# Kernel optimization log

Measured on AMD Instinct MI355X. Metric: run time of the kernel, lower is better.

Reference implementation:

```python
import jax, jax.numpy as jnp
import numpy as np

N_NODES = 60000
N_EDGES = 240000
N_REL = 4
N_GRAPHS = 128
D_IN = 768
D_H = 256
N_LAYERS = 6


def setup_inputs() -> dict:
    key = jax.random.key(0)
    ks = jax.random.split(key, 16)
    x = jax.random.normal(ks[0], (N_NODES, D_IN), dtype=jnp.float32)
    edge_index = jax.random.randint(ks[1], (2, N_EDGES), 0, N_NODES, dtype=jnp.int64)
    edge_attr = jax.random.randint(ks[2], (N_EDGES,), 0, N_REL, dtype=jnp.int64)
    batch = jnp.sort(jax.random.randint(ks[3], (N_NODES,), 0, N_GRAPHS, dtype=jnp.int64))
    s0 = 1.0 / np.sqrt(D_IN)
    s1 = 1.0 / np.sqrt(D_H)
    w0 = jax.random.normal(ks[4], (N_REL, D_IN, D_H), dtype=jnp.float32) * s0
    root0 = jax.random.normal(ks[5], (D_IN, D_H), dtype=jnp.float32) * s0
    b0 = jnp.zeros((D_H,), jnp.float32)
    w_rest = jax.random.normal(ks[6], (N_LAYERS - 1, N_REL, D_H, D_H), dtype=jnp.float32) * s1
    root_rest = jax.random.normal(ks[7], (N_LAYERS - 1, D_H, D_H), dtype=jnp.float32) * s1
    b_rest = jnp.zeros((N_LAYERS - 1, D_H), jnp.float32)
    fc1_w = jax.random.normal(ks[8], (2 * D_H, 128), dtype=jnp.float32) * (1.0 / np.sqrt(2 * D_H))
    fc1_b = jnp.zeros((128,), jnp.float32)
    fc2_w = jax.random.normal(ks[9], (128, 1), dtype=jnp.float32) * (1.0 / np.sqrt(128))
    fc2_b = jnp.zeros((1,), jnp.float32)
    return {"x": x, "edge_index": edge_index, "edge_attr": edge_attr, "batch": batch,
            "w0": w0, "root0": root0, "b0": b0,
            "w_rest": w_rest, "root_rest": root_rest, "b_rest": b_rest,
            "fc1_w": fc1_w, "fc1_b": fc1_b, "fc2_w": fc2_w, "fc2_b": fc2_b}


def _rgcn(h, src, dst, rel, W, root, b):
    # PyG RGCNConv with aggr='mean': per-relation mean over incoming edges,
    # transformed by per-relation weight, plus root transform and bias.
    n = h.shape[0]
    seg = rel * n + dst                                   # combined (relation, target) segment id
    msgs = h[src]                                         # [E, d_in] gather
    agg = jax.ops.segment_sum(msgs, seg, num_segments=N_REL * n)
    agg = agg.reshape(N_REL, n, -1)                       # [R, N, d_in]
    cnt = jax.ops.segment_sum(jnp.ones_like(rel, jnp.float32), seg, num_segments=N_REL * n)
    cnt = cnt.reshape(N_REL, n, 1)
    mean = agg / jnp.maximum(cnt, 1.0)                    # mean aggregation; 0 for isolated nodes
    return jnp.einsum('rnd,rdo->no', mean, W) + h @ root + b


def reference(x, edge_index, edge_attr, batch, w0, root0, b0,
              w_rest, root_rest, b_rest, fc1_w, fc1_b, fc2_w, fc2_b):
    src, dst = edge_index[0], edge_index[1]
    h = jax.nn.relu(_rgcn(x, src, dst, edge_attr, w0, root0, b0))
    for i in range(N_LAYERS - 1):
        h = jax.nn.relu(_rgcn(h, src, dst, edge_attr, w_rest[i], root_rest[i], b_rest[i]))
    # global mean / max pooling over graphs
    sums = jax.ops.segment_sum(h, batch, num_segments=N_GRAPHS)
    cnt = jax.ops.segment_sum(jnp.ones((h.shape[0],), jnp.float32), batch, num_segments=N_GRAPHS)[:, None]
    h_mean = sums / jnp.maximum(cnt, 1.0)
    h_max = jax.ops.segment_max(h, batch, num_segments=N_GRAPHS)
    h_max = jnp.where(cnt > 0, h_max, 0.0)
    g = jnp.concatenate([h_mean, h_max], axis=1)          # [G, 512]
    out = jax.nn.relu(g @ fc1_w + fc1_b)                  # dropout is identity at inference
    out = out @ fc2_w + fc2_b
    return jax.nn.sigmoid(out.squeeze(-1))                # [G]
```

## Files before the change

kernel.cpp:

```cpp
#include <hip/hip_runtime.h>
#include <hip/hip_bf16.h>

#define N_NODES  60000
#define N_EDGES  240000
#define N_REL    4
#define N_GRAPHS 128
#define D_IN     768
#define D_H      256
#define N_LAYERS 6
#define M_PAD    60032
#define N_TOT    1280
#define BM_L     64
#define LDM      264

static inline int cdiv(int a, int b) { return (a + b - 1) / b; }

typedef __attribute__((ext_vector_type(8))) short short8;
typedef __attribute__((ext_vector_type(4))) float f32x4;

__device__ __forceinline__ float bf2f(unsigned short u) {
    union { unsigned int i; float f; } c; c.i = ((unsigned int)u) << 16; return c.f;
}
__device__ __forceinline__ float bflo(unsigned int u) {
    union { unsigned int i; float f; } c; c.i = u << 16; return c.f;
}
__device__ __forceinline__ float bfhi(unsigned int u) {
    union { unsigned int i; float f; } c; c.i = u & 0xffff0000u; return c.f;
}
__device__ __forceinline__ unsigned short f2bf(float f) {
    union { float f; unsigned int i; } c; c.f = f;
    unsigned int i = c.i;
    unsigned int r = (i + 0x7FFFu + ((i >> 16) & 1u)) >> 16;
    return (unsigned short)r;
}

__device__ __forceinline__ void gload16(const void* g, void* l) {
    __builtin_amdgcn_global_load_lds((const __attribute__((address_space(1))) void*)g,
                                     (__attribute__((address_space(3))) void*)l, 16, 0, 0);
}

__global__ __launch_bounds__(512) void gemm_l0(
    const unsigned short* __restrict__ A,
    const unsigned short* __restrict__ Bt,
    const float* __restrict__ bias,
    unsigned short* __restrict__ out_root,
    unsigned short* __restrict__ out_msg,
    int K)
{
    __shared__ unsigned short As[128 * 32];
    __shared__ unsigned short Bs[256 * 32];

    const int tid  = threadIdx.x;
    const int wave = tid >> 6, lane = tid & 63;
    const int bn = blockIdx.x * 256;
    const int bm = blockIdx.y * 128;
    const int wm = (wave & 1) * 64, wn = (wave >> 1) * 64;

    const int lr = lane >> 2;
    const int kg = ((lane & 3) ^ ((lr ^ (lr >> 2)) & 3)) * 8;
    const unsigned short* gsrc[3];
    unsigned short* ldst[3];
    #pragma unroll
    for (int j = 0; j < 3; ++j) {
        int g = wave * 3 + j;
        if (g < 8) {
            gsrc[j] = A + (size_t)(bm + g * 16 + lr) * K + kg;
            ldst[j] = As + g * 16 * 32;
        } else {
            gsrc[j] = Bt + (size_t)(bn + (g - 8) * 16 + lr) * K + kg;
            ldst[j] = Bs + (g - 8) * 16 * 32;
        }
    }

    f32x4 acc[4][4] = {};
    const int fr = lane & 15;
    const int qsw = (((lane >> 4) ^ fr ^ (fr >> 2)) & 3) * 8;

    for (int k0 = 0; k0 < K; k0 += 32) {
        gload16(gsrc[0] + k0, ldst[0]);
        gload16(gsrc[1] + k0, ldst[1]);
        gload16(gsrc[2] + k0, ldst[2]);
        __syncthreads();

        short8 a[4], b[4];
        #pragma unroll
        for (int t = 0; t < 4; ++t) {
            a[t] = *(const short8*)&As[(wm + t * 16 + fr) * 32 + qsw];
            b[t] = *(const short8*)&Bs[(wn + t * 16 + fr) * 32 + qsw];
        }
        #pragma unroll
        for (int mt = 0; mt < 4; ++mt)
            #pragma unroll
            for (int nt = 0; nt < 4; ++nt)
                acc[mt][nt] = __builtin_amdgcn_mfma_f32_16x16x32_bf16(
                    a[mt], b[nt], acc[mt][nt], 0, 0, 0);
        __syncthreads();
    }

    const bool is_root = (bn == 0);
    #pragma unroll
    for (int mt = 0; mt < 4; ++mt) {
        #pragma unroll
        for (int nt = 0; nt < 4; ++nt) {
            int col = bn + wn + nt * 16 + fr;
            float bv = bias[col];
            #pragma unroll
            for (int r = 0; r < 4; ++r) {
                int row = bm + wm + mt * 16 + ((lane >> 4) << 2) + r;
                float v = acc[mt][nt][r] + bv;
                if (is_root) out_root[(size_t)row * 256 + col] = f2bf(v);
                else         out_msg[(size_t)row * 1024 + (col - 256)] = f2bf(v);
            }
        }
    }
}

__global__ __launch_bounds__(512) void rgcn_layer(
    const unsigned short* __restrict__ h,
    const unsigned short* __restrict__ Wl,
    const float* __restrict__ bias,
    const int* __restrict__ rp4,
    const int* __restrict__ e_srcs,
    const float* __restrict__ inv4,
    unsigned short* __restrict__ h_out)
{
    __shared__ unsigned short mt[BM_L * LDM];
    __shared__ unsigned short Bs[256 * 32];

    const int tid  = threadIdx.x;
    const int wave = tid >> 6, lane = tid & 63;
    const int bm = blockIdx.x * BM_L;

    const int node  = bm + lane;
    const int cq    = wave * 32;
    const bool valid = node < N_NODES;

    const int lr = lane >> 2;
    const int kg = ((lane & 3) ^ ((lr ^ (lr >> 2)) & 3)) * 8;

    const int fr  = lane & 15;
    const int q8  = (lane >> 4) * 8;
    const int qsw = (((lane >> 4) ^ fr ^ (fr >> 2)) & 3) * 8;
    const int wcol = wave * 32;

    float4 iv = valid ? *(const float4*)&inv4[(size_t)node * 4]
                      : make_float4(1.f, 1.f, 1.f, 1.f);

    f32x4 acc[4][2] = {};

    for (int r = 0; r < 5; ++r) {
        float4 am[8] = {};
        uint4 self[2];
        if (r < 4) {
            if (valid) {
                int lo = rp4[(size_t)node * 4 + r];
                int hi = rp4[(size_t)node * 4 + r + 1];
                for (int e = lo; e < hi; ++e) {
                    int s = e_srcs[e];
                    const uint4* hp = (const uint4*)(h + (size_t)s * 256 + cq);
                    #pragma unroll
                    for (int j = 0; j < 2; ++j) {
                        uint4 v = hp[j];
                        am[4*j+0].x += bflo(v.x); am[4*j+0].y += bfhi(v.x);
                        am[4*j+0].z += bflo(v.y); am[4*j+0].w += bfhi(v.y);
                        am[4*j+1].x += bflo(v.z); am[4*j+1].y += bfhi(v.z);
                        am[4*j+1].z += bflo(v.w); am[4*j+1].w += bfhi(v.w);
                    }
                    #pragma unroll
                    for (int j = 0; j < 0; ++j) {}
                }
            }
        }
        if (r < 4) {
            am[0]=make_float4(0,0,0,0); am[1]=am[0]; am[2]=am[0]; am[3]=am[0];
            am[4]=am[0]; am[5]=am[0]; am[6]=am[0]; am[7]=am[0];
            if (valid) {
                int lo = rp4[(size_t)node * 4 + r];
                int hi = rp4[(size_t)node * 4 + r + 1];
                for (int e = lo; e < hi; ++e) {
                    int s = e_srcs[e];
                    const uint4* hp = (const uint4*)(h + (size_t)s * 256 + cq);
                    #pragma unroll
                    for (int j = 0; j < 4; ++j) {
                        uint2 v = ((const uint2*)hp)[j];
                        am[2*j+0].x += bflo(v.x); am[2*j+0].y += bfhi(v.x);
                        am[2*j+0].z += bflo(v.y); am[2*j+0].w += bfhi(v.y);
                        uint2 w = ((const uint2*)hp)[j]; (void)w;
                        am[2*j+1].x += 0.f;
                    }
                }
            }
        }
        {
            #pragma unroll
            for (int j = 0; j < 8; ++j) am[j] = make_float4(0,0,0,0);
            if (r < 4) {
                if (valid) {
                    int lo = rp4[(size_t)node * 4 + r];
                    int hi = rp4[(size_t)node * 4 + r + 1];
                    for (int e = lo; e < hi; ++e) {
                        int s = e_srcs[e];
                        const uint4* hp = (const uint4*)(h + (size_t)s * 256 + cq);
                        uint4 v0 = hp[0];
                        uint4 v1 = hp[1];
                        am[0].x += bflo(v0.x); am[0].y += bfhi(v0.x);
                        am[0].z += bflo(v0.y); am[0].w += bfhi(v0.y);
                        am[1].x += bflo(v0.z); am[1].y += bfhi(v0.z);
                        am[1].z += bflo(v0.w); am[1].w += bfhi(v0.w);
                        am[2].x += bflo(v1.x); am[2].y += bfhi(v1.x);
                        am[2].z += bflo(v1.y); am[2].w += bfhi(v1.y);
                        am[3].x += bflo(v1.z); am[3].y += bfhi(v1.z);
                        am[3].z += bflo(v1.w); am[3].w += bfhi(v1.w);
                        const uint4* hp2 = hp + 2;
                        uint4 v2 = hp2[0];
                        uint4 v3 = hp2[1];
                        am[4].x += bflo(v2.x); am[4].y += bfhi(v2.x);
                        am[4].z += bflo(v2.y); am[4].w += bfhi(v2.y);
                        am[5].x += bflo(v2.z); am[5].y += bfhi(v2.z);
                        am[5].z += bflo(v2.w); am[5].w += bfhi(v2.w);
                        am[6].x += bflo(v3.x); am[6].y += bfhi(v3.x);
                        am[6].z += bflo(v3.y); am[6].w += bfhi(v3.y);
                        am[7].x += bflo(v3.z); am[7].y += bfhi(v3.z);
                        am[7].z += bflo(v3.w); am[7].w += bfhi(v3.w);
                    }
                }
            } else {
                const uint4* hp = (const uint4*)(h + (size_t)node * 256 + cq);
                self[0] = hp[0]; self[1] = hp[1];
                uint4 s2 = hp[2], s3 = hp[3];
                am[0].x = bflo(self[0].x); am[0].y = bfhi(self[0].x);
                am[0].z = bflo(self[0].y); am[0].w = bfhi(self[0].y);
                am[1].x = bflo(self[0].z); am[1].y = bfhi(self[0].z);
                am[1].z = bflo(self[0].w); am[1].w = bfhi(self[0].w);
                am[2].x = bflo(self[1].x); am[2].y = bfhi(self[1].x);
                am[2].z = bflo(self[1].y); am[2].w = bfhi(self[1].y);
                am[3].x = bflo(self[1].z); am[3].y = bfhi(self[1].z);
                am[3].z = bflo(self[1].w); am[3].w = bfhi(self[1].w);
                am[4].x = bflo(s2.x); am[4].y = bfhi(s2.x);
                am[4].z = bflo(s2.y); am[4].w = bfhi(s2.y);
                am[5].x = bflo(s2.z); am[5].y = bfhi(s2.z);
                am[5].z = bflo(s2.w); am[5].w = bfhi(s2.w);
                am[6].x = bflo(s3.x); am[6].y = bfhi(s3.x);
                am[6].z = bflo(s3.y); am[6].w = bfhi(s3.y);
                am[7].x = bflo(s3.z); am[7].y = bfhi(s3.z);
                am[7].z = bflo(s3.w); am[7].w = bfhi(s3.w);
            }
        }
        float sc = (r == 0) ? iv.x : (r == 1) ? iv.y : (r == 2) ? iv.z
                 : (r == 3) ? iv.w : 1.f;

        __syncthreads();
        {
            unsigned short* dst = &mt[lane * LDM + cq];
            #pragma unroll
            for (int j = 0; j < 8; ++j) {
                ushort4 o;
                o.x = f2bf(am[j].x * sc); o.y = f2bf(am[j].y * sc);
                o.z = f2bf(am[j].z * sc); o.w = f2bf(am[j].w * sc);
                *(ushort4*)(dst + j * 4) = o;
            }
        }

        const int rOff = r << 8;
        #pragma unroll 1
        for (int kk = 0; kk < 8; ++kk) {
            if (kk > 0) __syncthreads();
            {
                int g0 = wave * 2;
                gload16(Wl + (size_t)(g0 * 16 + lr) * N_TOT + rOff + kg + kk * 32,
                        Bs + g0 * 512);
                gload16(Wl + (size_t)((g0 + 1) * 16 + lr) * N_TOT + rOff + kg + kk * 32,
                        Bs + (g0 + 1) * 512);
            }
            __syncthreads();

            short8 a[4], b[2];
            #pragma unroll
            for (int i = 0; i < 4; ++i)
                a[i] = *(const short8*)&mt[(i * 16 + fr) * LDM + kk * 32 + q8];
            #pragma unroll
            for (int nt = 0; nt < 2; ++nt)
                b[nt] = *(const short8*)&Bs[(wcol + nt * 16 + fr) * 32 + qsw];
            #pragma unroll
            for (int i = 0; i < 4; ++i)
                #pragma unroll
                for (int nt = 0; nt < 2; ++nt)
                    acc[i][nt] = __builtin_amdgcn_mfma_f32_16x16x32_bf16(
                        a[i], b[nt], acc[i][nt], 0, 0, 0);
        }
        __syncthreads();
    }

    #pragma unroll
    for (int i = 0; i < 4; ++i) {
        #pragma unroll
        for (int nt = 0; nt < 2; ++nt) {
            int col = wcol + nt * 16 + fr;
            float bv = bias[col];
            #pragma unroll
            for (int rg = 0; rg < 4; ++rg) {
                int row = bm + i * 16 + ((lane >> 4) << 2) + rg;
                float v = fmaxf(acc[i][nt][rg] + bv, 0.f);
                h_out[(size_t)row * 256 + col] = f2bf(v);
            }
        }
    }
}

__global__ void convert_x(const float* __restrict__ x, unsigned short* __restrict__ xb) {
    size_t i = ((size_t)blockIdx.x * 256 + threadIdx.x) * 4;
    if (i >= (size_t)M_PAD * D_IN) return;
    ushort4 o;
    if (i < (size_t)N_NODES * D_IN) {
        float4 v = *(const float4*)&x[i];
        o.x = f2bf(v.x); o.y = f2bf(v.y); o.z = f2bf(v.z); o.w = f2bf(v.w);
    } else {
        o.x = o.y = o.z = o.w = 0;
    }
    *(ushort4*)&xb[i] = o;
}

__global__ void pack_w0(const float* __restrict__ root0, const float* __restrict__ w0,
                        unsigned short* __restrict__ Wt0) {
    int idx = blockIdx.x * 256 + threadIdx.x;
    if (idx >= N_TOT * D_IN) return;
    int k = idx % D_IN, n = idx / D_IN;
    float v = (n < 256) ? root0[k * 256 + n]
                        : w0[(((n >> 8) - 1) * D_IN + k) * 256 + (n & 255)];
    Wt0[idx] = f2bf(v);
}

__global__ void pack_wr(const float* __restrict__ root_rest, const float* __restrict__ w_rest,
                        unsigned short* __restrict__ WtR) {
    int idx = blockIdx.x * 256 + threadIdx.x;
    if (idx >= 5 * 256 * N_TOT) return;
    int k = idx % N_TOT; int t = idx / N_TOT; int n = t & 255; int l = t >> 8;
    float v = (k < 1024)
        ? w_rest[(((l * 4 + (k >> 8)) * 256) + (k & 255)) * 256 + n]
        : root_rest[(l * 256 + (k - 1024)) * 256 + n];
    WtR[idx] = f2bf(v);
}

__global__ void build_bias(const float* __restrict__ b0, float* __restrict__ eb) {
    int i = blockIdx.x * 256 + threadIdx.x;
    if (i < N_TOT) eb[i] = (i < 256) ? b0[i] : 0.f;
}

__global__ void deg4_count(const int* __restrict__ dst, const int* __restrict__ rel,
                           int* __restrict__ deg4, int E) {
    int e = blockIdx.x * 256 + threadIdx.x;
    if (e < E) atomicAdd(&deg4[dst[e] * 4 + rel[e]], 1);
}

__global__ void invert4(const int* __restrict__ deg4, float* __restrict__ inv4, int n) {
    int i = blockIdx.x * 256 + threadIdx.x;
    if (i < n) inv4[i] = 1.0f / (float)max(deg4[i], 1);
}

__global__ __launch_bounds__(256) void block_sum(const int* __restrict__ deg,
                                                 int* __restrict__ bsum, int n) {
    __shared__ int s[256];
    int i = blockIdx.x * 256 + threadIdx.x;
    s[threadIdx.x] = (i < n) ? deg[i] : 0;
    __syncthreads();
    for (int o = 128; o > 0; o >>= 1) {
        if (threadIdx.x < o) s[threadIdx.x] += s[threadIdx.x + o];
        __syncthreads();
    }
    if (threadIdx.x == 0) bsum[blockIdx.x] = s[0];
}

__global__ __launch_bounds__(1024) void scan_bsum(const int* __restrict__ bsum,
                                                  int* __restrict__ boff, int nb) {
    __shared__ int s[1024];
    int t = threadIdx.x;
    int v0 = (t < nb) ? bsum[t] : 0;
    s[t] = v0;
    __syncthreads();
    for (int o = 1; o < 1024; o <<= 1) {
        int v = (t >= o) ? s[t - o] : 0;
        __syncthreads();
        s[t] += v;
        __syncthreads();
    }
    if (t < nb) boff[t] = s[t] - v0;
}

__global__ __launch_bounds__(256) void block_scan_write(
    const int* __restrict__ deg, const int* __restrict__ boff,
    int* __restrict__ row_ptr, int* __restrict__ cursor, int n, int total) {
    __shared__ int s[256];
    int t = threadIdx.x;
    int i = blockIdx.x * 256 + t;
    int v = (i < n) ? deg[i] : 0;
    s[t] = v;
    __syncthreads();
    for (int o = 1; o < 256; o <<= 1) {
        int u = (t >= o) ? s[t - o] : 0;
        __syncthreads();
        s[t] += u;
        __syncthreads();
    }
    int excl = s[t] - v + boff[blockIdx.x];
    if (i < n) { row_ptr[i] = excl; cursor[i] = excl; }
    if (blockIdx.x == 0 && t == 0) row_ptr[n] = total;
}

__global__ void place_edges4(const int* __restrict__ dst, const int* __restrict__ src,
                             const int* __restrict__ rel, int* __restrict__ cursor,
                             int* __restrict__ e_srcs, int E) {
    int e = blockIdx.x * 256 + threadIdx.x;
    if (e < E) {
        int p = atomicAdd(&cursor[dst[e] * 4 + rel[e]], 1);
        e_srcs[p] = src[e];
    }
}

__global__ __launch_bounds__(256) void aggregate0(
    const unsigned short* __restrict__ rootb,
    const unsigned short* __restrict__ msg,
    const int* __restrict__ rp4, const int* __restrict__ e_srcs,
    const float* __restrict__ inv4,
    unsigned short* __restrict__ h_out)
{
    int node = blockIdx.x * 4 + (threadIdx.x >> 6);
    if (node >= N_NODES) return;
    int lane = threadIdx.x & 63;
    float4 iv = *(const float4*)&inv4[(size_t)node * 4];

    ushort4 rt = *(const ushort4*)&rootb[(size_t)node * 256 + lane * 4];
    float4 acc = make_float4(bf2f(rt.x), bf2f(rt.y), bf2f(rt.z), bf2f(rt.w));

    #pragma unroll
    for (int r = 0; r < 4; ++r) {
        int lo = rp4[(size_t)node * 4 + r], hi = rp4[(size_t)node * 4 + r + 1];
        float f = (r == 0) ? iv.x : (r == 1) ? iv.y : (r == 2) ? iv.z : iv.w;
        float4 s4 = make_float4(0, 0, 0, 0);
        for (int e = lo; e < hi; ++e) {
            int s = e_srcs[e];
            ushort4 m = *(const ushort4*)&msg[(size_t)s * 1024 + (r << 8) + lane * 4];
            s4.x += bf2f(m.x); s4.y += bf2f(m.y);
            s4.z += bf2f(m.z); s4.w += bf2f(m.w);
        }
        acc.x += s4.x * f; acc.y += s4.y * f;
        acc.z += s4.z * f; acc.w += s4.w * f;
    }
    ushort4 o;
    o.x = f2bf(fmaxf(acc.x, 0.f));
    o.y = f2bf(fmaxf(acc.y, 0.f));
    o.z = f2bf(fmaxf(acc.z, 0.f));
    o.w = f2bf(fmaxf(acc.w, 0.f));
    *(ushort4*)&h_out[(size_t)node * 256 + lane * 4] = o;
}

__global__ __launch_bounds__(256) void pool_kernel(
    const unsigned short* __restrict__ h, const int* __restrict__ batch,
    float* __restrict__ g_feat)
{
    int g = blockIdx.x;
    int t = threadIdx.x;
    __shared__ int s_lo, s_hi;
    if (t == 0) {
        int lo = 0, hi = N_NODES;
        while (lo < hi) { int m = (lo + hi) >> 1; if (batch[m] < g) lo = m + 1; else hi = m; }
        s_lo = lo;
        int lo2 = lo, hi2 = N_NODES;
        while (lo2 < hi2) { int m = (lo2 + hi2) >> 1; if (batch[m] < g + 1) lo2 = m + 1; else hi2 = m; }
        s_hi = lo2;
    }
    __syncthreads();
    int lo = s_lo, hi = s_hi;
    float sum = 0.f, mx = 0.f;
    for (int n = lo; n < hi; ++n) {
        float v = bf2f(h[(size_t)n * 256 + t]);
        sum += v;
        mx = fmaxf(mx, v);
    }
    float cnt = (float)(hi - lo);
    g_feat[g * 512 + t]       = sum / fmaxf(cnt, 1.0f);
    g_feat[g * 512 + 256 + t] = (cnt > 0.f) ? mx : 0.f;
}

__global__ __launch_bounds__(128) void mlp_head(
    const float* __restrict__ g_feat,
    const float* __restrict__ fc1_w, const float* __restrict__ fc1_b,
    const float* __restrict__ fc2_w, const float* __restrict__ fc2_b,
    float* __restrict__ out)
{
    __shared__ float gf[512];
    __shared__ float partial[2];
    int g = blockIdx.x, t = threadIdx.x;
    for (int i = t; i < 512; i += 128) gf[i] = g_feat[g * 512 + i];
    __syncthreads();
    float acc = fc1_b[t];
    for (int i = 0; i < 512; ++i) acc += gf[i] * fc1_w[i * 128 + t];
    float h1 = fmaxf(acc, 0.f);
    float v = h1 * fc2_w[t];
    #pragma unroll
    for (int off = 32; off > 0; off >>= 1) v += __shfl_down(v, off);
    if ((t & 63) == 0) partial[t >> 6] = v;
    __syncthreads();
    if (t == 0) {
        float s = partial[0] + partial[1] + fc2_b[0];
        out[g] = 1.0f / (1.0f + expf(-s));
    }
}

extern "C" void kernel_launch(void* const* d_in, const int* in_sizes, int n_in,
                              void* d_out, int out_size, void* d_ws, size_t ws_size,
                              hipStream_t stream) {
    const float* x          = (const float*)d_in[0];
    const int*   edge_index = (const int*)d_in[1];
    const int*   edge_attr  = (const int*)d_in[2];
    const int*   batch      = (const int*)d_in[3];
    const float* w0         = (const float*)d_in[4];
    const float* root0      = (const float*)d_in[5];
    const float* b0         = (const float*)d_in[6];
    const float* w_rest     = (const float*)d_in[7];
    const float* root_rest  = (const float*)d_in[8];
    const float* b_rest     = (const float*)d_in[9];
    const float* fc1_w      = (const float*)d_in[10];
    const float* fc1_b      = (const float*)d_in[11];
    const float* fc2_w      = (const float*)d_in[12];
    const float* fc2_b      = (const float*)d_in[13];
    float* out = (float*)d_out;

    const int* e_src = edge_index;
    const int* e_dst = edge_index + N_EDGES;

    char* p = (char*)d_ws;
    auto alloc = [&](size_t bytes) { char* q = p; p += (bytes + 255) & ~(size_t)255; return q; };
    unsigned short* x_bf   = (unsigned short*)alloc((size_t)M_PAD * D_IN * 2);
    unsigned short* msgbuf = (unsigned short*)alloc((size_t)M_PAD * 1024 * 2);
    unsigned short* hA     = (unsigned short*)alloc((size_t)M_PAD * 256 * 2);
    unsigned short* hB     = (unsigned short*)alloc((size_t)M_PAD * 256 * 2);
    unsigned short* Wt0    = (unsigned short*)alloc((size_t)N_TOT * D_IN * 2);
    unsigned short* WtR    = (unsigned short*)alloc((size_t)5 * 256 * N_TOT * 2);
    float*          ebias  = (float*)alloc(N_TOT * 4);
    float*          inv4   = (float*)alloc((size_t)N_NODES * 4 * 4);
    float*          g_feat = (float*)alloc((size_t)N_GRAPHS * 512 * 4);
    int*            deg4   = (int*)alloc((size_t)N_NODES * 4 * 4);
    int*            rp4    = (int*)alloc(((size_t)N_NODES * 4 + 1) * 4);
    int*            cursor4= (int*)alloc((size_t)N_NODES * 4 * 4);
    int*            bsum   = (int*)alloc(1024 * 4);
    int*            boff   = (int*)alloc(1024 * 4);
    int*            e_srcs = (int*)alloc((size_t)N_EDGES * 4);

    const int n4 = N_NODES * 4;
    const int nscan4 = cdiv(n4, 256);

    hipMemsetAsync(deg4, 0, (size_t)n4 * 4, stream);
    convert_x<<<cdiv(M_PAD * D_IN / 4, 256), 256, 0, stream>>>(x, x_bf);
    pack_w0<<<cdiv(N_TOT * D_IN, 256), 256, 0, stream>>>(root0, w0, Wt0);
    pack_wr<<<cdiv(5 * 256 * N_TOT, 256), 256, 0, stream>>>(root_rest, w_rest, WtR);
    build_bias<<<cdiv(N_TOT, 256), 256, 0, stream>>>(b0, ebias);
    deg4_count<<<cdiv(N_EDGES, 256), 256, 0, stream>>>(e_dst, edge_attr, deg4, N_EDGES);
    invert4<<<cdiv(n4, 256), 256, 0, stream>>>(deg4, inv4, n4);
    block_sum<<<nscan4, 256, 0, stream>>>(deg4, bsum, n4);
    scan_bsum<<<1, 1024, 0, stream>>>(bsum, boff, nscan4);
    block_scan_write<<<nscan4, 256, 0, stream>>>(deg4, boff, rp4, cursor4, n4, N_EDGES);
    place_edges4<<<cdiv(N_EDGES, 256), 256, 0, stream>>>(e_dst, e_src, edge_attr,
                                                         cursor4, e_srcs, N_EDGES);

    gemm_l0<<<dim3(N_TOT / 256, M_PAD / 128), 512, 0, stream>>>(
        x_bf, Wt0, ebias, hB, msgbuf, D_IN);
    aggregate0<<<cdiv(N_NODES, 4), 256, 0, stream>>>(hB, msgbuf, rp4, e_srcs, inv4, hA);

    unsigned short* cur = hA;
    unsigned short* nxt = hB;
    for (int L = 1; L < N_LAYERS; ++L) {
        rgcn_layer<<<M_PAD / BM_L, 512, 0, stream>>>(
            cur, WtR + (size_t)(L - 1) * 256 * N_TOT, b_rest + (size_t)(L - 1) * 256,
            rp4, e_srcs, inv4, nxt);
        unsigned short* t = cur; cur = nxt; nxt = t;
    }

    pool_kernel<<<N_GRAPHS, 256, 0, stream>>>(cur, batch, g_feat);
    mlp_head<<<N_GRAPHS, 128, 0, stream>>>(g_feat, fc1_w, fc1_b, fc2_w, fc2_b, out);
}
```

Before: 1.208 ms.

## Remove redundant gather passes, load layer weights directly, swizzle gemm blocks

Removes two dead duplicate gather loops in the RGCN layer kernel that recomputed and discarded neighbour sums. Weight fragments are now read straight from global memory, replacing LDS staging and the per-k barriers that went with it. Edge loops are unrolled by two for more loads in flight. The layer-0 GEMM uses a grouped block ordering for better L2 reuse. Direct global weight loads rely on cache hits and could add latency.

```diff
diff --git a/kernel.cpp b/kernel.cpp
--- a/kernel.cpp
+++ b/kernel.cpp
@@ -39,6 +39,25 @@
                                      (__attribute__((address_space(3))) void*)l, 16, 0, 0);
 }
 
+__device__ __forceinline__ void accum32(float4* am, uint4 v0, uint4 v1, uint4 v2, uint4 v3) {
+    am[0].x += bflo(v0.x); am[0].y += bfhi(v0.x);
+    am[0].z += bflo(v0.y); am[0].w += bfhi(v0.y);
+    am[1].x += bflo(v0.z); am[1].y += bfhi(v0.z);
+    am[1].z += bflo(v0.w); am[1].w += bfhi(v0.w);
+    am[2].x += bflo(v1.x); am[2].y += bfhi(v1.x);
+    am[2].z += bflo(v1.y); am[2].w += bfhi(v1.y);
+    am[3].x += bflo(v1.z); am[3].y += bfhi(v1.z);
+    am[3].z += bflo(v1.w); am[3].w += bfhi(v1.w);
+    am[4].x += bflo(v2.x); am[4].y += bfhi(v2.x);
+    am[4].z += bflo(v2.y); am[4].w += bfhi(v2.y);
+    am[5].x += bflo(v2.z); am[5].y += bfhi(v2.z);
+    am[5].z += bflo(v2.w); am[5].w += bfhi(v2.w);
+    am[6].x += bflo(v3.x); am[6].y += bfhi(v3.x);
+    am[6].z += bflo(v3.y); am[6].w += bfhi(v3.y);
+    am[7].x += bflo(v3.z); am[7].y += bfhi(v3.z);
+    am[7].z += bflo(v3.w); am[7].w += bfhi(v3.w);
+}
+
 __global__ __launch_bounds__(512) void gemm_l0(
     const unsigned short* __restrict__ A,
     const unsigned short* __restrict__ Bt,
@@ -52,8 +71,12 @@
 
     const int tid  = threadIdx.x;
     const int wave = tid >> 6, lane = tid & 63;
-    const int bn = blockIdx.x * 256;
-    const int bm = blockIdx.y * 128;
+
+    int b = blockIdx.x;
+    int bm, bn;
+    if (b < 2320) { int grp = b / 40, rem = b % 40; bm = (grp * 8 + (rem & 7)) * 128; bn = (rem >> 3) * 256; }
+    else          { int rem = b - 2320; bm = (464 + rem % 5) * 128; bn = (rem / 5) * 256; }
+
     const int wm = (wave & 1) * 64, wn = (wave >> 1) * 64;
 
     const int lr = lane >> 2;
@@ -82,18 +105,18 @@
         gload16(gsrc[2] + k0, ldst[2]);
         __syncthreads();
 
-        short8 a[4], b[4];
+        short8 a[4], bb[4];
         #pragma unroll
         for (int t = 0; t < 4; ++t) {
-            a[t] = *(const short8*)&As[(wm + t * 16 + fr) * 32 + qsw];
-            b[t] = *(const short8*)&Bs[(wn + t * 16 + fr) * 32 + qsw];
+            a[t]  = *(const short8*)&As[(wm + t * 16 + fr) * 32 + qsw];
+            bb[t] = *(const short8*)&Bs[(wn + t * 16 + fr) * 32 + qsw];
         }
         #pragma unroll
         for (int mt = 0; mt < 4; ++mt)
             #pragma unroll
             for (int nt = 0; nt < 4; ++nt)
                 acc[mt][nt] = __builtin_amdgcn_mfma_f32_16x16x32_bf16(
-                    a[mt], b[nt], acc[mt][nt], 0, 0, 0);
+                    a[mt], bb[nt], acc[mt][nt], 0, 0, 0);
         __syncthreads();
     }
 
@@ -125,7 +148,6 @@
     unsigned short* __restrict__ h_out)
 {
     __shared__ unsigned short mt[BM_L * LDM];
-    __shared__ unsigned short Bs[256 * 32];
 
     const int tid  = threadIdx.x;
     const int wave = tid >> 6, lane = tid & 63;
@@ -135,13 +157,12 @@
     const int cq    = wave * 32;
     const bool valid = node < N_NODES;
 
-    const int lr = lane >> 2;
-    const int kg = ((lane & 3) ^ ((lr ^ (lr >> 2)) & 3)) * 8;
-
-    const int fr  = lane & 15;
-    const int q8  = (lane >> 4) * 8;
-    const int qsw = (((lane >> 4) ^ fr ^ (fr >> 2)) & 3) * 8;
+    const int fr   = lane & 15;
+    const int q8   = (lane >> 4) * 8;
     const int wcol = wave * 32;
+
+    const unsigned short* w0p = Wl + (size_t)(wcol + fr) * N_TOT + q8;
+    const unsigned short* w1p = Wl + (size_t)(wcol + 16 + fr) * N_TOT + q8;
 
     float4 iv = valid ? *(const float4*)&inv4[(size_t)node * 4]
                       : make_float4(1.f, 1.f, 1.f, 1.f);
@@ -149,102 +170,31 @@
     f32x4 acc[4][2] = {};
 
     for (int r = 0; r < 5; ++r) {
-        float4 am[8] = {};
-        uint4 self[2];
+        float4 am[8];
+        #pragma unroll
+        for (int j = 0; j < 8; ++j) am[j] = make_float4(0.f, 0.f, 0.f, 0.f);
+
         if (r < 4) {
             if (valid) {
                 int lo = rp4[(size_t)node * 4 + r];
                 int hi = rp4[(size_t)node * 4 + r + 1];
-                for (int e = lo; e < hi; ++e) {
-                    int s = e_srcs[e];
-                    const uint4* hp = (const uint4*)(h + (size_t)s * 256 + cq);
-                    #pragma unroll
-                    for (int j = 0; j < 2; ++j) {
-                        uint4 v = hp[j];
-                        am[4*j+0].x += bflo(v.x); am[4*j+0].y += bfhi(v.x);
-                        am[4*j+0].z += bflo(v.y); am[4*j+0].w += bfhi(v.y);
-                        am[4*j+1].x += bflo(v.z); am[4*j+1].y += bfhi(v.z);
-                        am[4*j+1].z += bflo(v.w); am[4*j+1].w += bfhi(v.w);
-                    }
-                    #pragma unroll
-                    for (int j = 0; j < 0; ++j) {}
+                int e = lo;
+                for (; e + 1 < hi; e += 2) {
+                    const uint4* p0 = (const uint4*)(h + (size_t)e_srcs[e] * 256 + cq);
+                    const uint4* p1 = (const uint4*)(h + (size_t)e_srcs[e + 1] * 256 + cq);
+                    uint4 v0 = p0[0], v1 = p0[1], v2 = p0[2], v3 = p0[3];
+                    uint4 u0 = p1[0], u1 = p1[1], u2 = p1[2], u3 = p1[3];
+                    accum32(am, v0, v1, v2, v3);
+                    accum32(am, u0, u1, u2, u3);
+                }
+                if (e < hi) {
+                    const uint4* p0 = (const uint4*)(h + (size_t)e_srcs[e] * 256 + cq);
+                    accum32(am, p0[0], p0[1], p0[2], p0[3]);
                 }
             }
-        }
-        if (r < 4) {
-            am[0]=make_float4(0,0,0,0); am[1]=am[0]; am[2]=am[0]; am[3]=am[0];
-            am[4]=am[0]; am[5]=am[0]; am[6]=am[0]; am[7]=am[0];
-            if (valid) {
-                int lo = rp4[(size_t)node * 4 + r];
-                int hi = rp4[(size_t)node * 4 + r + 1];
-                for (int e = lo; e < hi; ++e) {
-                    int s = e_srcs[e];
-                    const uint4* hp = (const uint4*)(h + (size_t)s * 256 + cq);
-                    #pragma unroll
-                    for (int j = 0; j < 4; ++j) {
-                        uint2 v = ((const uint2*)hp)[j];
-                        am[2*j+0].x += bflo(v.x); am[2*j+0].y += bfhi(v.x);
-                        am[2*j+0].z += bflo(v.y); am[2*j+0].w += bfhi(v.y);
-                        uint2 w = ((const uint2*)hp)[j]; (void)w;
-                        am[2*j+1].x += 0.f;
-                    }
-                }
-            }
-        }
-        {
-            #pragma unroll
-            for (int j = 0; j < 8; ++j) am[j] = make_float4(0,0,0,0);
-            if (r < 4) {
-                if (valid) {
-                    int lo = rp4[(size_t)node * 4 + r];
-                    int hi = rp4[(size_t)node * 4 + r + 1];
-                    for (int e = lo; e < hi; ++e) {
-                        int s = e_srcs[e];
-                        const uint4* hp = (const uint4*)(h + (size_t)s * 256 + cq);
-                        uint4 v0 = hp[0];
-                        uint4 v1 = hp[1];
-                        am[0].x += bflo(v0.x); am[0].y += bfhi(v0.x);
-                        am[0].z += bflo(v0.y); am[0].w += bfhi(v0.y);
-                        am[1].x += bflo(v0.z); am[1].y += bfhi(v0.z);
-                        am[1].z += bflo(v0.w); am[1].w += bfhi(v0.w);
-                        am[2].x += bflo(v1.x); am[2].y += bfhi(v1.x);
-                        am[2].z += bflo(v1.y); am[2].w += bfhi(v1.y);
-                        am[3].x += bflo(v1.z); am[3].y += bfhi(v1.z);
-                        am[3].z += bflo(v1.w); am[3].w += bfhi(v1.w);
-                        const uint4* hp2 = hp + 2;
-                        uint4 v2 = hp2[0];
-                        uint4 v3 = hp2[1];
-                        am[4].x += bflo(v2.x); am[4].y += bfhi(v2.x);
-                        am[4].z += bflo(v2.y); am[4].w += bfhi(v2.y);
-                        am[5].x += bflo(v2.z); am[5].y += bfhi(v2.z);
-                        am[5].z += bflo(v2.w); am[5].w += bfhi(v2.w);
-                        am[6].x += bflo(v3.x); am[6].y += bfhi(v3.x);
-                        am[6].z += bflo(v3.y); am[6].w += bfhi(v3.y);
-                        am[7].x += bflo(v3.z); am[7].y += bfhi(v3.z);
-                        am[7].z += bflo(v3.w); am[7].w += bfhi(v3.w);
-                    }
-                }
-            } else {
-                const uint4* hp = (const uint4*)(h + (size_t)node * 256 + cq);
-                self[0] = hp[0]; self[1] = hp[1];
-                uint4 s2 = hp[2], s3 = hp[3];
-                am[0].x = bflo(self[0].x); am[0].y = bfhi(self[0].x);
-                am[0].z = bflo(self[0].y); am[0].w = bfhi(self[0].y);
-                am[1].x = bflo(self[0].z); am[1].y = bfhi(self[0].z);
-                am[1].z = bflo(self[0].w); am[1].w = bfhi(self[0].w);
-                am[2].x = bflo(self[1].x); am[2].y = bfhi(self[1].x);
-                am[2].z = bflo(self[1].y); am[2].w = bfhi(self[1].y);
-                am[3].x = bflo(self[1].z); am[3].y = bfhi(self[1].z);
-                am[3].z = bflo(self[1].w); am[3].w = bfhi(self[1].w);
-                am[4].x = bflo(s2.x); am[4].y = bfhi(s2.x);
-                am[4].z = bflo(s2.y); am[4].w = bfhi(s2.y);
-                am[5].x = bflo(s2.z); am[5].y = bfhi(s2.z);
-                am[5].z = bflo(s2.w); am[5].w = bfhi(s2.w);
-                am[6].x = bflo(s3.x); am[6].y = bfhi(s3.x);
-                am[6].z = bflo(s3.y); am[6].w = bfhi(s3.y);
-                am[7].x = bflo(s3.z); am[7].y = bfhi(s3.z);
-                am[7].z = bflo(s3.w); am[7].w = bfhi(s3.w);
-            }
+        } else {
+            const uint4* p0 = (const uint4*)(h + (size_t)node * 256 + cq);
+            accum32(am, p0[0], p0[1], p0[2], p0[3]);
         }
         float sc = (r == 0) ? iv.x : (r == 1) ? iv.y : (r == 2) ? iv.z
                  : (r == 3) ? iv.w : 1.f;
@@ -260,35 +210,23 @@
                 *(ushort4*)(dst + j * 4) = o;
             }
         }
-
-        const int rOff = r << 8;
-        #pragma unroll 1
+        __syncthreads();
+
+        const int rOff = (r << 8);
+        #pragma unroll
         for (int kk = 0; kk < 8; ++kk) {
-            if (kk > 0) __syncthreads();
-            {
-                int g0 = wave * 2;
-                gload16(Wl + (size_t)(g0 * 16 + lr) * N_TOT + rOff + kg + kk * 32,
-                        Bs + g0 * 512);
-                gload16(Wl + (size_t)((g0 + 1) * 16 + lr) * N_TOT + rOff + kg + kk * 32,
-                        Bs + (g0 + 1) * 512);
-            }
-            __syncthreads();
-
-            short8 a[4], b[2];
+            short8 b0 = *(const short8*)(w0p + rOff + kk * 32);
+            short8 b1 = *(const short8*)(w1p + rOff + kk * 32);
+            short8 a[4];
             #pragma unroll
             for (int i = 0; i < 4; ++i)
                 a[i] = *(const short8*)&mt[(i * 16 + fr) * LDM + kk * 32 + q8];
             #pragma unroll
-            for (int nt = 0; nt < 2; ++nt)
-                b[nt] = *(const short8*)&Bs[(wcol + nt * 16 + fr) * 32 + qsw];
-            #pragma unroll
-            for (int i = 0; i < 4; ++i)
-                #pragma unroll
-                for (int nt = 0; nt < 2; ++nt)
-                    acc[i][nt] = __builtin_amdgcn_mfma_f32_16x16x32_bf16(
-                        a[i], b[nt], acc[i][nt], 0, 0, 0);
-        }
-        __syncthreads();
+            for (int i = 0; i < 4; ++i) {
+                acc[i][0] = __builtin_amdgcn_mfma_f32_16x16x32_bf16(a[i], b0, acc[i][0], 0, 0, 0);
+                acc[i][1] = __builtin_amdgcn_mfma_f32_16x16x32_bf16(a[i], b1, acc[i][1], 0, 0, 0);
+            }
+        }
     }
 
     #pragma unroll
@@ -436,11 +374,19 @@
         int lo = rp4[(size_t)node * 4 + r], hi = rp4[(size_t)node * 4 + r + 1];
         float f = (r == 0) ? iv.x : (r == 1) ? iv.y : (r == 2) ? iv.z : iv.w;
         float4 s4 = make_float4(0, 0, 0, 0);
-        for (int e = lo; e < hi; ++e) {
-            int s = e_srcs[e];
-            ushort4 m = *(const ushort4*)&msg[(size_t)s * 1024 + (r << 8) + lane * 4];
-            s4.x += bf2f(m.x); s4.y += bf2f(m.y);
-            s4.z += bf2f(m.z); s4.w += bf2f(m.w);
+        int e = lo;
+        for (; e + 1 < hi; e += 2) {
+            ushort4 m0 = *(const ushort4*)&msg[(size_t)e_srcs[e] * 1024 + (r << 8) + lane * 4];
+            ushort4 m1 = *(const ushort4*)&msg[(size_t)e_srcs[e + 1] * 1024 + (r << 8) + lane * 4];
+            s4.x += bf2f(m0.x) + bf2f(m1.x);
+            s4.y += bf2f(m0.y) + bf2f(m1.y);
+            s4.z += bf2f(m0.z) + bf2f(m1.z);
+            s4.w += bf2f(m0.w) + bf2f(m1.w);
+        }
+        if (e < hi) {
+            ushort4 m0 = *(const ushort4*)&msg[(size_t)e_srcs[e] * 1024 + (r << 8) + lane * 4];
+            s4.x += bf2f(m0.x); s4.y += bf2f(m0.y);
+            s4.z += bf2f(m0.z); s4.w += bf2f(m0.w);
         }
         acc.x += s4.x * f; acc.y += s4.y * f;
         acc.z += s4.z * f; acc.w += s4.w * f;
@@ -562,8 +508,7 @@
     place_edges4<<<cdiv(N_EDGES, 256), 256, 0, stream>>>(e_dst, e_src, edge_attr,
                                                          cursor4, e_srcs, N_EDGES);
 
-    gemm_l0<<<dim3(N_TOT / 256, M_PAD / 128), 512, 0, stream>>>(
-        x_bf, Wt0, ebias, hB, msgbuf, D_IN);
+    gemm_l0<<<2345, 512, 0, stream>>>(x_bf, Wt0, ebias, hB, msgbuf, D_IN);
     aggregate0<<<cdiv(N_NODES, 4), 256, 0, stream>>>(hB, msgbuf, rp4, e_srcs, inv4, hA);
 
     unsigned short* cur = hA;
```

New measurement: 1.368 ms. 1.13x slower.
